# Kernel tuning notes

Hardware: AMD Instinct MI355X
Metric: run time of the kernel (lower is better)

Reference implementation:

```python
import jax, jax.numpy as jnp
import numpy as np

B, IN_C, OUT_C, H, W = 16, 64, 64, 128, 128
MIN_R, MAX_R, BASE, SCALE = 1, 6, 3, 3


def setup_inputs() -> dict:
    key = jax.random.key(0)
    k1, k2 = jax.random.split(key)
    x = jax.random.normal(k1, (B, IN_C, H, W), dtype=jnp.float32)
    # kaiming-uniform-ish scale for a 3x3 conv weight
    weight = jax.random.normal(k2, (OUT_C, IN_C, 3, 3), dtype=jnp.float32) * (1.0 / np.sqrt(IN_C * 9))
    # truncated-normal-style integer dilation per output channel (deterministic)
    rng = np.random.default_rng(0)
    offsets = np.clip(np.round(rng.normal(BASE, SCALE, size=OUT_C)), MIN_R, MAX_R).astype(np.int32)
    return {"x": x, "weight": weight, "offsets": offsets}


def _gsd_conv(x, weight, offs_np):
    # Per-channel dilation conv: group channels by dilation, conv each group
    # (dilation=o, padding=o keeps HxW), scatter back to original channel order.
    out = jnp.zeros((x.shape[0], weight.shape[0], x.shape[2], x.shape[3]), dtype=x.dtype)
    for o in np.unique(offs_np):
        idx = np.nonzero(offs_np == o)[0]          # static channel indices for this dilation
        w = weight[idx]                             # [g, in_c, 3, 3]
        o = int(o)
        y = jax.lax.conv_general_dilated(
            x, w,
            window_strides=(1, 1),
            padding=[(o, o), (o, o)],
            rhs_dilation=(o, o),
            dimension_numbers=("NCHW", "OIHW", "NCHW"),
        )                                           # [B, g, H, W]
        out = out.at[:, idx].set(y)
    return out


def reference(x, weight, offsets):
    offs_np = np.asarray(offsets)
    return _gsd_conv(x, weight, offs_np)
```

## Files before the change

### kernel.cpp

```cpp
#include <hip/hip_runtime.h>


#define HW_ 128
#define C_ 64
#define B_ 16
#define EX 44
#define EY 28
#define NPIX (EY * EX)
#define NCHUNK (NPIX * 2)
#define NSETS 39
#define BUFDW (NSETS * 64 * 4)
#define PADW 140
#define PLANE_STRIDE (PADW * PADW * 16)
#define MAX_ITEMS 12
#define WS_WPACK_OFF 1024
#define WS_XB16_OFF (1 << 20)
#define XB16_BYTES ((size_t)B_ * 4 * PLANE_STRIDE * 2)


typedef __attribute__((ext_vector_type(8))) short short8;
typedef __attribute__((ext_vector_type(16))) float floatx16;

__device__ __forceinline__ unsigned bf16rne(float f) {
  unsigned u = __float_as_uint(f);
  return (u + 0x7FFFu + ((u >> 16) & 1u)) >> 16;
}

#define GLOAD_LDS16(g, l)                                   \
  __builtin_amdgcn_global_load_lds(                         \
      (const __attribute__((address_space(1))) void*)(g),   \
      (__attribute__((address_space(3))) void*)(l), 16, 0, 0)

__global__ __launch_bounds__(256) void gsd_prep(
    const float* __restrict__ x, const int* __restrict__ offsets,
    const float* __restrict__ w, int* __restrict__ desc,
    uint4* __restrict__ wpack, unsigned short* __restrict__ xb16,
    const int nrow) {
  const int bid = blockIdx.x;
  const int tid = threadIdx.x;

  if (bid < nrow) {
    const int b = bid / PADW, py = bid - b * PADW;
    uint4* o4 = (uint4*)xb16;
    const size_t pb0 = ((size_t)b * 4) * 39200 + (size_t)py * 280;
    const uint4 z = make_uint4(0, 0, 0, 0);
    if (py < 6 || py >= PADW - 6) {
      for (int i = tid; i < 1120; i += 256) {
        const int ks = i / 280, r = i - ks * 280;
        o4[pb0 + (size_t)ks * 39200 + r] = z;
      }
      return;
    }
    if (tid < 96) {
      const int ks = tid / 24, rr = tid - ks * 24;
      const int idx = rr < 12 ? rr : 256 + rr;
      o4[pb0 + (size_t)ks * 39200 + idx] = z;
    }
    const int y = py - 6;
    __shared__ unsigned l32[128 * 33];
    const int xx = tid & 127, ph = tid >> 7;
    const float* xp = x + (size_t)b * (C_ * HW_ * HW_) + y * HW_ + xx;
#pragma unroll 4
    for (int p = ph; p < 32; p += 2) {
      const float v0 = xp[(2 * p) * (HW_ * HW_)];
      const float v1 = xp[(2 * p + 1) * (HW_ * HW_)];
      l32[xx * 33 + p] = bf16rne(v0) | (bf16rne(v1) << 16);
    }
    __syncthreads();
#pragma unroll 4
    for (int ch = tid; ch < 1024; ch += 256) {
      const int ks = ch >> 8, r = ch & 255;
      const unsigned* s = &l32[(r >> 1) * 33 + ks * 8 + (r & 1) * 4];
      o4[pb0 + (size_t)ks * 39200 + 12 + r] = make_uint4(s[0], s[1], s[2], s[3]);
    }
    return;
  }

  __shared__ int sd[128];
  __shared__ int soffs[C_];
  if (tid < C_) soffs[tid] = offsets[tid];
  __syncthreads();
  if (tid < C_) {
    const int key = soffs[tid];
    int rank = 0;
    for (int c = 0; c < C_; ++c) {
      const int kc = soffs[c];
      rank += (int)((kc < key) | ((kc == key) & (c < tid)));
    }
    sd[rank] = tid;
  }
  __syncthreads();
  if (tid == 0) {
    int ni = 0;
    for (int t = 0; t < 2; ++t) {
      int cnt = 0, prev = -1;
      for (int m = 0; m < 32; ++m) {
        const int dd = soffs[sd[t * 32 + m]];
        if (dd != prev && cnt < 6 && ni < MAX_ITEMS) {
          sd[66 + t * 6 + cnt] = dd;
          sd[78 + t * 6 + cnt] = ni;
          sd[91 + ni * 2] = t;
          sd[92 + ni * 2] = dd;
          ++ni;
          ++cnt;
          prev = dd;
        }
      }
      sd[64 + t] = cnt;
    }
    sd[90] = ni;
  }
  __syncthreads();

  const int sbid = bid - nrow;
  if (sbid == 0) {
    if (tid < 91) desc[tid] = sd[tid];
    return;
  }
  const int wix = sbid - 1;
  if (wix >= sd[90]) return;
  const int o = sd[91 + wix * 2];
  const int dit = sd[92 + wix * 2];

  for (int i = tid; i < 4 * 9 * 64; i += 256) {
    const int ks = i / 576;
    const int r = i % 576;
    const int tap = r >> 6;
    const int lane = r & 63;
    const int m = lane & 31, hh = lane >> 5;
    const int oc = sd[o * 32 + m];
    const bool act = (soffs[oc] == dit);
    unsigned ww[4];
    for (int jj = 0; jj < 4; ++jj) {
      float v0 = 0.f, v1 = 0.f;
      if (act) {
        const int ic0 = ks * 16 + hh * 8 + jj * 2;
        v0 = w[(oc * C_ + ic0) * 9 + tap];
        v1 = w[(oc * C_ + ic0 + 1) * 9 + tap];
      }
      ww[jj] = bf16rne(v0) | (bf16rne(v1) << 16);
    }
    wpack[(size_t)wix * 2304 + i] = make_uint4(ww[0], ww[1], ww[2], ww[3]);
  }
}

template <bool PRE>
__global__ __launch_bounds__(512, 4) void gsd_conv(
    const float* __restrict__ x, const unsigned short* __restrict__ xb16,
    const int* __restrict__ desc, const uint4* __restrict__ wpack,
    float* __restrict__ out) {
  const int tid = threadIdx.x;
  const int bid0 = blockIdx.x;
  const int gxid = (bid0 & 7) * 64 + (bid0 >> 3);
  const int b = gxid >> 5;
  const int yt = (gxid >> 2) & 7;
  const int xt = gxid & 3;
  const int y0 = yt * 16, x0 = xt * 32;

  const int lane = tid & 63;
  const int n = lane & 31;
  const int h = lane >> 5;
  const int wv = tid >> 6;
  const int o = wv >> 2;
  const int rq = wv & 3;

  __shared__ __align__(16) unsigned ldsbuf[2][BUFDW];

  floatx16 acc[4];
#pragma unroll
  for (int rt = 0; rt < 4; ++rt)
#pragma unroll
    for (int e = 0; e < 16; ++e) acc[rt][e] = 0.f;

  const unsigned short* xbase;
  int srcoff[5];
  if constexpr (PRE) {
    xbase = xb16 + (size_t)b * 4 * PLANE_STRIDE;
#pragma unroll
    for (int j = 0; j < 5; ++j) {
      const int q = (wv + j * 8) * 64 + lane;
      int pix = q >> 1;
      if (pix > NPIX - 1) pix = NPIX - 1;
      const int p = q & 1;
      const int yy = pix / EX, xx = pix - yy * EX;
      const int half = p ^ ((pix >> 2) & 1);
      srcoff[j] = ((y0 + yy) * PADW + (x0 + xx)) * 16 + half * 8;
    }
  }
  int slx, sq, sy2, gxc;
  bool xin;
  const float* xb;
  if constexpr (!PRE) {
    slx = tid & 63;
    sq = (tid >> 6) & 3;
    sy2 = tid >> 8;
    xb = x + (size_t)b * (C_ * HW_ * HW_);
    const int gx = x0 - 6 + slx;
    gxc = gx < 0 ? 0 : (gx > 127 ? 127 : gx);
    xin = ((unsigned)gx < 128u) & (slx < EX);
  }

  const int cnt = __builtin_amdgcn_readfirstlane(desc[64 + o]);

  auto STAGE = [&](int buf, int ks) {
    if constexpr (PRE) {
      const unsigned short* xp = xbase + (size_t)ks * PLANE_STRIDE;
#pragma unroll
      for (int j = 0; j < 5; ++j) {
        if (j < 4) {
          GLOAD_LDS16(xp + srcoff[j], &ldsbuf[buf][(wv + j * 8) * 256]);
        } else if (wv < 7) {
          GLOAD_LDS16(xp + srcoff[4], &ldsbuf[buf][(wv + 32) * 256]);
        }
      }
    }
  };

  auto COMPUTE = [&](const unsigned* cbuf, int ks) {
    for (int s = 0; s < cnt; ++s) {
      const int d = __builtin_amdgcn_readfirstlane(desc[66 + o * 6 + s]);
      const int wix = __builtin_amdgcn_readfirstlane(desc[78 + o * 6 + s]);
      const uint4* wp = wpack + ((size_t)wix * 4 + ks) * 576 + lane;
#pragma unroll
      for (int tap = 0; tap < 9; ++tap) {
        const int ky = tap / 3 - 1, kx = tap % 3 - 1;
        const short8 af = __builtin_bit_cast(short8, wp[tap * 64]);
        const int pybase = rq * 4 + ky * d + 6;
        const int pxb = n + kx * d + 6;
#pragma unroll
        for (int rt = 0; rt < 4; ++rt) {
          const int pix = (pybase + rt) * EX + pxb;
          const int dws = (pix << 3) + ((h ^ ((pix >> 2) & 1)) << 2);
          const short8 bf = *reinterpret_cast<const short8*>(&cbuf[dws]);
          acc[rt] = __builtin_amdgcn_mfma_f32_32x32x16_bf16(af, bf, acc[rt],
                                                            0, 0, 0);
        }
      }
    }
  };

  if constexpr (PRE) {
    STAGE(0, 0);
    __syncthreads();
#pragma unroll
    for (int ks = 0; ks < 3; ++ks) {
      STAGE((ks + 1) & 1, ks + 1);
      COMPUTE(ldsbuf[ks & 1], ks);
      __syncthreads();
    }
    COMPUTE(ldsbuf[1], 3);
  } else {
    for (int ks = 0; ks < 4; ++ks) {
      if (ks) __syncthreads();
      const float* xp = xb + (size_t)(ks * 16 + sq * 4) * (HW_ * HW_);
#pragma unroll 2
      for (int yy = sy2; yy < EY; yy += 2) {
        const int gy = y0 - 6 + yy;
        const int gyc = gy < 0 ? 0 : (gy > 127 ? 127 : gy);
        const bool ok = xin & ((unsigned)gy < 128u);
        const float* p = xp + gyc * HW_ + gxc;
        float v0 = p[0];
        float v1 = p[HW_ * HW_];
        float v2 = p[2 * HW_ * HW_];
        float v3 = p[3 * HW_ * HW_];
        if (!ok) { v0 = v1 = v2 = v3 = 0.f; }
        const unsigned lo = bf16rne(v0) | (bf16rne(v1) << 16);
        const unsigned hi = bf16rne(v2) | (bf16rne(v3) << 16);
        if (slx < EX) {
          const int pix = yy * EX + slx;
          const int dws =
              pix * 8 + (((sq >> 1) ^ ((pix >> 2) & 1)) << 2) + ((sq & 1) << 1);
          *reinterpret_cast<uint2*>(&ldsbuf[0][dws]) = make_uint2(lo, hi);
        }
      }
      __syncthreads();
      COMPUTE(ldsbuf[0], ks);
    }
  }

  int oc[16];
#pragma unroll
  for (int reg = 0; reg < 16; ++reg) {
    const int row = (reg & 3) + 8 * (reg >> 2) + 4 * h;
    oc[reg] = desc[o * 32 + row];
  }
#pragma unroll
  for (int rt = 0; rt < 4; ++rt) {
    const int y = y0 + rq * 4 + rt;
#pragma unroll
    for (int reg = 0; reg < 16; ++reg) {
      out[((size_t)(b * C_ + oc[reg]) * HW_ + y) * HW_ + x0 + n] =
          acc[rt][reg];
    }
  }
}

extern "C" void kernel_launch(void* const* d_in, const int* in_sizes, int n_in,
                              void* d_out, int out_size, void* d_ws,
                              size_t ws_size, hipStream_t stream) {
  const float* x = (const float*)d_in[0];
  const float* w = (const float*)d_in[1];
  const int* offsets = (const int*)d_in[2];
  float* out = (float*)d_out;

  int* desc = (int*)d_ws;
  uint4* wpack = (uint4*)((char*)d_ws + WS_WPACK_OFF);
  unsigned short* xb16 = (unsigned short*)((char*)d_ws + WS_XB16_OFF);

  const bool pre = ws_size >= (size_t)WS_XB16_OFF + XB16_BYTES;
  const int nrow = pre ? B_ * PADW : 0;

  gsd_prep<<<dim3(nrow + 1 + MAX_ITEMS), 256, 0, stream>>>(
      x, offsets, w, desc, wpack, xb16, nrow);
  if (pre) {
    gsd_conv<true><<<dim3(B_ * 8 * 4), 512, 0, stream>>>(
        x, xb16, desc, wpack, out);
  } else {
    gsd_conv<false><<<dim3(B_ * 8 * 4), 512, 0, stream>>>(
        x, xb16, desc, wpack, out);
  }
}
```

Baseline: 185.1 us.

## Group output channels by dilation into shared items across all waves

Work items are rebuilt as runs of up to 32 channels that share one dilation, instead of one item per dilation within each fixed 32-channel half. Every wave now processes all items for two output rows, rather than one half of the channels for four rows. This cuts the MFMAs wasted on zero-padded weight rows, since items no longer repeat a dilation across both halves. In exchange, each wave keeps a much larger accumulator array (7 items × 2 rows), which may raise register pressure or cause spills under the existing launch bounds.

```diff
diff --git a/kernel.cpp b/kernel.cpp
--- a/kernel.cpp
+++ b/kernel.cpp
@@ -7,12 +7,12 @@
 #define EX 44
 #define EY 28
 #define NPIX (EY * EX)
-#define NCHUNK (NPIX * 2)
 #define NSETS 39
 #define BUFDW (NSETS * 64 * 4)
 #define PADW 140
 #define PLANE_STRIDE (PADW * PADW * 16)
 #define MAX_ITEMS 12
+#define ITEMS_MAX 7
 #define WS_WPACK_OFF 1024
 #define WS_XB16_OFF (1 << 20)
 #define XB16_BYTES ((size_t)B_ * 4 * PLANE_STRIDE * 2)
@@ -91,36 +91,32 @@
   }
   __syncthreads();
   if (tid == 0) {
-    int ni = 0;
-    for (int t = 0; t < 2; ++t) {
-      int cnt = 0, prev = -1;
-      for (int m = 0; m < 32; ++m) {
-        const int dd = soffs[sd[t * 32 + m]];
-        if (dd != prev && cnt < 6 && ni < MAX_ITEMS) {
-          sd[66 + t * 6 + cnt] = dd;
-          sd[78 + t * 6 + cnt] = ni;
-          sd[91 + ni * 2] = t;
-          sd[92 + ni * 2] = dd;
-          ++ni;
-          ++cnt;
-          prev = dd;
-        }
-      }
-      sd[64 + t] = cnt;
-    }
-    sd[90] = ni;
+    int ni = 0, c = 0;
+    while (c < C_ && ni < MAX_ITEMS) {
+      const int d = soffs[sd[c]];
+      int e = c;
+      while (e < C_ && soffs[sd[e]] == d) ++e;
+      for (int st = c; st < e && ni < MAX_ITEMS; st += 32) {
+        sd[66 + ni] = d;
+        sd[78 + ni] = st;
+        sd[90 + ni] = (e - st) < 32 ? (e - st) : 32;
+        ++ni;
+      }
+      c = e;
+    }
+    sd[64] = ni;
   }
   __syncthreads();
 
   const int sbid = bid - nrow;
   if (sbid == 0) {
-    if (tid < 91) desc[tid] = sd[tid];
+    if (tid < 102) desc[tid] = sd[tid];
     return;
   }
   const int wix = sbid - 1;
-  if (wix >= sd[90]) return;
-  const int o = sd[91 + wix * 2];
-  const int dit = sd[92 + wix * 2];
+  if (wix >= sd[64]) return;
+  const int start = sd[78 + wix];
+  const int g = sd[90 + wix];
 
   for (int i = tid; i < 4 * 9 * 64; i += 256) {
     const int ks = i / 576;
@@ -128,8 +124,8 @@
     const int tap = r >> 6;
     const int lane = r & 63;
     const int m = lane & 31, hh = lane >> 5;
-    const int oc = sd[o * 32 + m];
-    const bool act = (soffs[oc] == dit);
+    const bool act = m < g;
+    const int oc = act ? sd[start + m] : 0;
     unsigned ww[4];
     for (int jj = 0; jj < 4; ++jj) {
       float v0 = 0.f, v1 = 0.f;
@@ -161,16 +157,17 @@
   const int n = lane & 31;
   const int h = lane >> 5;
   const int wv = tid >> 6;
-  const int o = wv >> 2;
-  const int rq = wv & 3;
+  const int yb = wv * 2;
 
   __shared__ __align__(16) unsigned ldsbuf[2][BUFDW];
 
-  floatx16 acc[4];
-#pragma unroll
-  for (int rt = 0; rt < 4; ++rt)
-#pragma unroll
-    for (int e = 0; e < 16; ++e) acc[rt][e] = 0.f;
+  floatx16 acc[ITEMS_MAX][2];
+#pragma unroll
+  for (int s = 0; s < ITEMS_MAX; ++s)
+#pragma unroll
+    for (int rt = 0; rt < 2; ++rt)
+#pragma unroll
+      for (int e = 0; e < 16; ++e) acc[s][rt][e] = 0.f;
 
   const unsigned short* xbase;
   int srcoff[5];
@@ -200,7 +197,7 @@
     xin = ((unsigned)gx < 128u) & (slx < EX);
   }
 
-  const int cnt = __builtin_amdgcn_readfirstlane(desc[64 + o]);
+  const int cnt = __builtin_amdgcn_readfirstlane(desc[64]);
 
   auto STAGE = [&](int buf, int ks) {
     if constexpr (PRE) {
@@ -217,23 +214,25 @@
   };
 
   auto COMPUTE = [&](const unsigned* cbuf, int ks) {
-    for (int s = 0; s < cnt; ++s) {
-      const int d = __builtin_amdgcn_readfirstlane(desc[66 + o * 6 + s]);
-      const int wix = __builtin_amdgcn_readfirstlane(desc[78 + o * 6 + s]);
-      const uint4* wp = wpack + ((size_t)wix * 4 + ks) * 576 + lane;
-#pragma unroll
-      for (int tap = 0; tap < 9; ++tap) {
-        const int ky = tap / 3 - 1, kx = tap % 3 - 1;
-        const short8 af = __builtin_bit_cast(short8, wp[tap * 64]);
-        const int pybase = rq * 4 + ky * d + 6;
-        const int pxb = n + kx * d + 6;
-#pragma unroll
-        for (int rt = 0; rt < 4; ++rt) {
-          const int pix = (pybase + rt) * EX + pxb;
-          const int dws = (pix << 3) + ((h ^ ((pix >> 2) & 1)) << 2);
-          const short8 bf = *reinterpret_cast<const short8*>(&cbuf[dws]);
-          acc[rt] = __builtin_amdgcn_mfma_f32_32x32x16_bf16(af, bf, acc[rt],
-                                                            0, 0, 0);
+#pragma unroll
+    for (int s = 0; s < ITEMS_MAX; ++s) {
+      if (s < cnt) {
+        const int d = __builtin_amdgcn_readfirstlane(desc[66 + s]);
+        const uint4* wp = wpack + ((size_t)s * 4 + ks) * 576 + lane;
+#pragma unroll
+        for (int tap = 0; tap < 9; ++tap) {
+          const int ky = tap / 3 - 1, kx = tap % 3 - 1;
+          const short8 af = __builtin_bit_cast(short8, wp[tap * 64]);
+          const int prow = yb + ky * d + 6;
+          const int pxb = n + kx * d + 6;
+#pragma unroll
+          for (int rt = 0; rt < 2; ++rt) {
+            const int pix = (prow + rt) * EX + pxb;
+            const int dws = (pix << 3) + ((h ^ ((pix >> 2) & 1)) << 2);
+            const short8 bf = *reinterpret_cast<const short8*>(&cbuf[dws]);
+            acc[s][rt] = __builtin_amdgcn_mfma_f32_32x32x16_bf16(
+                af, bf, acc[s][rt], 0, 0, 0);
+          }
         }
       }
     }
@@ -278,19 +277,23 @@
     }
   }
 
-  int oc[16];
-#pragma unroll
-  for (int reg = 0; reg < 16; ++reg) {
-    const int row = (reg & 3) + 8 * (reg >> 2) + 4 * h;
-    oc[reg] = desc[o * 32 + row];
-  }
-#pragma unroll
-  for (int rt = 0; rt < 4; ++rt) {
-    const int y = y0 + rq * 4 + rt;
-#pragma unroll
-    for (int reg = 0; reg < 16; ++reg) {
-      out[((size_t)(b * C_ + oc[reg]) * HW_ + y) * HW_ + x0 + n] =
-          acc[rt][reg];
+#pragma unroll
+  for (int s = 0; s < ITEMS_MAX; ++s) {
+    if (s < cnt) {
+      const int start = __builtin_amdgcn_readfirstlane(desc[78 + s]);
+      const int g = __builtin_amdgcn_readfirstlane(desc[90 + s]);
+#pragma unroll
+      for (int reg = 0; reg < 16; ++reg) {
+        const int row = (reg & 3) + 8 * (reg >> 2) + 4 * h;
+        if (row < g) {
+          const int oc = desc[start + row];
+#pragma unroll
+          for (int rt = 0; rt < 2; ++rt) {
+            out[((size_t)(b * C_ + oc) * HW_ + (y0 + yb + rt)) * HW_ + x0 + n] =
+                acc[s][rt][reg];
+          }
+        }
+      }
     }
   }
 }
```

Result: slower. 561.8 us (+203.5%).
